# Kernel tuning notes

Hardware: AMD Instinct MI355X
Metric: run time of the kernel (lower is better)

## Reference

```python
import jax, jax.numpy as jnp
import numpy as np

B, NQ, NK = 16, 512, 1024
CQ, CV = 128, 128
H, D = 8, 64            # nb_heads, attention_size
SCALE = float(np.sqrt(D))


def setup_inputs() -> dict:
    key = jax.random.key(0)
    ks = jax.random.split(key, 10)
    s = 0.02
    return {
        "query": jax.random.normal(ks[0], (B, NQ, CQ), jnp.float32),
        "key": jax.random.normal(ks[1], (B, NK, CV), jnp.float32),
        "c_mask": jax.random.randint(ks[2], (B, NK), 0, 2).astype(jnp.float32),
        # torch Linear params, stored as [in, out] so y = x @ W + b
        "Wq": jax.random.normal(ks[3], (CQ, H * D), jnp.float32) * s,
        "bq": jnp.zeros((H * D,), jnp.float32),
        "Wk": jax.random.normal(ks[4], (CV, H * D), jnp.float32) * s,
        "bk": jnp.zeros((H * D,), jnp.float32),
        "Wv": jax.random.normal(ks[5], (CV, H * D), jnp.float32) * s,
        "bv": jnp.zeros((H * D,), jnp.float32),
    }


def reference(query, key, c_mask, Wq, bq, Wk, bk, Wv, bv):
    # projections -> [B, N, H, D]
    q = (query @ Wq + bq).reshape(B, NQ, H, D)
    k = (key @ Wk + bk).reshape(B, NK, H, D)
    v = (key @ Wv + bv).reshape(B, NK, H, D)
    # scaled scores [B, H, NQ, NK]
    scores = jnp.einsum('bqhd,bkhd->bhqk', q / SCALE, k)
    # additive mask: c_mask [B, NK] broadcasts over heads and queries
    scores = scores - 100000.0 * (1.0 - c_mask[:, None, None, :])
    attn = jax.nn.softmax(scores, axis=-1)
    # weighted values -> [B, NQ, H, D] -> concat heads
    c = jnp.einsum('bhqk,bkhd->bqhd', attn, v)
    return c.reshape(B, NQ, H * D)
```

## Files before the change

kernel.cpp:

```cpp
#include <hip/hip_runtime.h>
#include <hip/hip_bf16.h>

#define B_  16
#define NQ_ 512
#define NK_ 1024
#define CQ_ 128
#define H_  8
#define D_  64
#define HD_ 512

typedef __attribute__((ext_vector_type(8))) short short8;
typedef __attribute__((ext_vector_type(4))) float floatx4;

__device__ __forceinline__ short f2bf(float f) {
    union { float f; unsigned u; } x; x.f = f;
    unsigned r = (x.u + 0x7fffu + ((x.u >> 16) & 1u)) >> 16;
    return (short)r;
}
__device__ __forceinline__ int f2bf_pk(float a, float b) {
    __hip_bfloat162 h = __float22bfloat162_rn(make_float2(a, b));
    int r; __builtin_memcpy(&r, &h, 4); return r;
}
__device__ __forceinline__ short8 pack8(float4 a, float4 b) {
    union { int4 i; short8 s; } u;
    u.i = make_int4(f2bf_pk(a.x, a.y), f2bf_pk(a.z, a.w),
                    f2bf_pk(b.x, b.y), f2bf_pk(b.z, b.w));
    return u.s;
}
__device__ __forceinline__ int2 packi2(floatx4 a) {
    return make_int2(f2bf_pk(a[0], a[1]), f2bf_pk(a[2], a[3]));
}
__device__ __forceinline__ void async16(const short* g, short* l) {
    __builtin_amdgcn_global_load_lds(
        (const __attribute__((address_space(1))) void*)g,
        (__attribute__((address_space(3))) void*)l, 16, 0, 0);
}

__global__ void prep_kernel(const float* __restrict__ W0, const float* __restrict__ W1,
                            const float* __restrict__ W2, short* __restrict__ T0,
                            short* __restrict__ T1, short* __restrict__ T2,
                            const float* __restrict__ bq, float* __restrict__ bqs,
                            float qscale) {
    int gi = blockIdx.x * blockDim.x + threadIdx.x;
    if (gi < 196608) {
        int sel = gi >> 16;
        int idx = gi & 65535;
        const float* W = sel == 0 ? W0 : (sel == 1 ? W1 : W2);
        short* T = sel == 0 ? T0 : (sel == 1 ? T1 : T2);
        float s = sel == 0 ? qscale : 1.0f;
        int n = idx >> 7, k = idx & 127;
        T[idx] = f2bf(W[k * HD_ + n] * s);
        return;
    }
    int j = gi - 196608;
    if (j < HD_) bqs[j] = bq[j] * qscale;
}

__global__ __launch_bounds__(256, 2) void kvproj_kernel(
    const float* __restrict__ key_,
    const short* __restrict__ wkt, const short* __restrict__ wvt,
    const float* __restrict__ bk, const float* __restrict__ bv,
    short* __restrict__ ks, short* __restrict__ vt)
{
    __shared__ __align__(16) short csh[9216];

    int bx = blockIdx.x;
    const short* Wt; const float* bias; short* out; int transposed;
    if (bx < 128) { Wt = wkt; bias = bk; out = ks; transposed = 0; }
    else { bx -= 128; Wt = wvt; bias = bv; out = vt; transposed = 1; }

    const int tid  = threadIdx.x;
    const int w    = tid >> 6, lane = tid & 63;
    const int l15  = lane & 15, quad = lane >> 4;
    const int mbase = bx * 128;

    short8 afr[2][4];
    #pragma unroll
    for (int mt = 0; mt < 2; ++mt) {
        const float* xrow = key_ + (size_t)(mbase + w * 32 + mt * 16 + l15) * CQ_;
        #pragma unroll
        for (int kt = 0; kt < 4; ++kt)
            afr[mt][kt] = pack8(*(const float4*)(xrow + kt * 32 + quad * 8),
                                *(const float4*)(xrow + kt * 32 + quad * 8 + 4));
    }

    const int b  = mbase >> 10;
    const int r0 = mbase & 1023;

    #pragma unroll
    for (int hh = 0; hh < 2; ++hh) {
        const int h = blockIdx.y * 2 + hh;
        short8 bfr[4][4];
        #pragma unroll
        for (int nt = 0; nt < 4; ++nt) {
            const short8* wrow = (const short8*)(Wt + (size_t)(h * 64 + nt * 16 + l15) * CQ_);
            #pragma unroll
            for (int kt = 0; kt < 4; ++kt) bfr[nt][kt] = wrow[kt * 4 + quad];
        }
        floatx4 acc[2][4];
        #pragma unroll
        for (int mt = 0; mt < 2; ++mt)
            #pragma unroll
            for (int nt = 0; nt < 4; ++nt) {
                floatx4 a = {0.f, 0.f, 0.f, 0.f};
                #pragma unroll
                for (int kt = 0; kt < 4; ++kt)
                    a = __builtin_amdgcn_mfma_f32_16x16x32_bf16(afr[mt][kt], bfr[nt][kt], a, 0, 0, 0);
                acc[mt][nt] = a;
            }
        __syncthreads();
        #pragma unroll
        for (int mt = 0; mt < 2; ++mt)
            #pragma unroll
            for (int nt = 0; nt < 4; ++nt) {
                const float bvv = bias[h * 64 + nt * 16 + l15];
                #pragma unroll
                for (int i = 0; i < 4; ++i) {
                    const short s = f2bf(acc[mt][nt][i] + bvv);
                    const int m = w * 32 + mt * 16 + quad * 4 + i;
                    const int n = nt * 16 + l15;
                    if (!transposed) csh[m * 72 + n]  = s;
                    else             csh[n * 136 + m] = s;
                }
            }
        __syncthreads();

        const size_t bh = (size_t)(b * H_ + h);
        if (!transposed) {
            short* dst = out + (bh * NK_ + r0) * D_;
            #pragma unroll
            for (int it = 0; it < 4; ++it) {
                const int idx = it * 256 + tid;
                const int row = idx >> 3, c8 = (idx & 7) * 8;
                *(short8*)(dst + idx * 8) = *(const short8*)&csh[row * 72 + c8];
            }
        } else {
            short* dst = out + bh * D_ * NK_ + r0;
            #pragma unroll
            for (int it = 0; it < 4; ++it) {
                const int idx = it * 256 + tid;
                const int row = idx >> 4, c8 = (idx & 15) * 8;
                *(short8*)(dst + (size_t)row * NK_ + c8) = *(const short8*)&csh[row * 136 + c8];
            }
        }
    }
}

__global__ __launch_bounds__(256, 2) void attn_kernel(
    const float* __restrict__ query, const short* __restrict__ ks,
    const short* __restrict__ vt, const float* __restrict__ cmask,
    const short* __restrict__ wqt, const float* __restrict__ bqs,
    float* __restrict__ out)
{
    __shared__ __align__(16) short kbuf[2][64 * 64];
    __shared__ __align__(16) short vbuf[2][64 * 64];
    __shared__ __align__(16) short psh[128 * 64];

    const int tid = threadIdx.x;
    const int w = tid >> 6, lane = tid & 63;
    const int l15 = lane & 15, quad = lane >> 4;

    const int bx   = blockIdx.x;
    const int bh_i = bx & 127;
    const int qq   = bx >> 7;
    const int h    = bh_i & 7;
    const int b    = bh_i >> 3;

    const size_t bh = (size_t)bh_i;
    const short* kb_ = ks + bh * NK_ * D_;
    const short* vb  = vt + bh * D_ * NK_;
    const float* mk  = cmask + (size_t)b * NK_;

    short8 qa[2][2];
    {
        short8 waf[4][4];
        #pragma unroll
        for (int dt = 0; dt < 4; ++dt)
            #pragma unroll
            for (int kt = 0; kt < 4; ++kt)
                waf[dt][kt] = *(const short8*)(wqt + (size_t)(h * 64 + dt * 16 + l15) * CQ_ + kt * 32 + quad * 8);
        const int qr0 = qq * 128 + w * 32;
        #pragma unroll
        for (int g = 0; g < 2; ++g) {
            const float* qrow = query + ((size_t)b * NQ_ + qr0 + g * 16 + l15) * CQ_;
            short8 bqf[4];
            #pragma unroll
            for (int kt = 0; kt < 4; ++kt)
                bqf[kt] = pack8(*(const float4*)(qrow + kt * 32 + quad * 8),
                                *(const float4*)(qrow + kt * 32 + quad * 8 + 4));
            const int prow = w * 32 + g * 16 + l15;
            #pragma unroll
            for (int dt = 0; dt < 4; ++dt) {
                float4 bi = *(const float4*)(bqs + h * 64 + dt * 16 + quad * 4);
                floatx4 a = {bi.x, bi.y, bi.z, bi.w};
                #pragma unroll
                for (int kt = 0; kt < 4; ++kt)
                    a = __builtin_amdgcn_mfma_f32_16x16x32_bf16(waf[dt][kt], bqf[kt], a, 0, 0, 0);
                const int c16 = (dt * 2 + (quad >> 1)) ^ (prow & 7);
                *(int2*)&psh[prow * 64 + c16 * 8 + (quad & 1) * 4] = packi2(a);
            }
            qa[g][0] = *(const short8*)&psh[prow * 64 + ((quad    ) ^ (prow & 7)) * 8];
            qa[g][1] = *(const short8*)&psh[prow * 64 + ((4 + quad) ^ (prow & 7)) * 8];
        }
    }

    const int srow8 = lane >> 3, sc = lane & 7;

    float l_lane[2] = {0.f, 0.f};
    floatx4 o_acc[2][4];
    #pragma unroll
    for (int g = 0; g < 2; ++g)
        #pragma unroll
        for (int dt = 0; dt < 4; ++dt) o_acc[g][dt] = (floatx4){0.f, 0.f, 0.f, 0.f};

    #pragma unroll
    for (int j = 0; j < 2; ++j) {
        const int row = w * 16 + j * 8 + srow8;
        const int cs = sc ^ (row & 7);
        async16(kb_ + (size_t)row * D_ + cs * 8, &kbuf[0][(w * 16 + j * 8) * 64]);
        async16(vb + (size_t)row * NK_ + cs * 8, &vbuf[0][(w * 16 + j * 8) * 64]);
    }
    __syncthreads();

    for (int t = 0; t < 16; ++t) {
        const int cur = t & 1;
        if (t < 15) {
            const int nb = (t + 1) * 64, nxt = cur ^ 1;
            #pragma unroll
            for (int j = 0; j < 2; ++j) {
                const int row = w * 16 + j * 8 + srow8;
                const int cs = sc ^ (row & 7);
                async16(kb_ + (size_t)(nb + row) * D_ + cs * 8, &kbuf[nxt][(w * 16 + j * 8) * 64]);
                async16(vb + (size_t)row * NK_ + nb + cs * 8, &vbuf[nxt][(w * 16 + j * 8) * 64]);
            }
        }
        const short* kb = kbuf[cur];
        const short* vbl = vbuf[cur];
        const int kbase = t * 64;

        short8 ka[4][2];
        #pragma unroll
        for (int nt = 0; nt < 4; ++nt) {
            const int row = nt * 16 + l15;
            ka[nt][0] = *(const short8*)&kb[row * 64 + ((quad    ) ^ (row & 7)) * 8];
            ka[nt][1] = *(const short8*)&kb[row * 64 + ((4 + quad) ^ (row & 7)) * 8];
        }
        short8 vf[2][4];
        #pragma unroll
        for (int dt = 0; dt < 4; ++dt) {
            const int row = dt * 16 + l15;
            vf[0][dt] = *(const short8*)&vbl[row * 64 + ((quad    ) ^ (row & 7)) * 8];
            vf[1][dt] = *(const short8*)&vbl[row * 64 + ((4 + quad) ^ (row & 7)) * 8];
        }
        float4 m4[4];
        #pragma unroll
        for (int nt = 0; nt < 4; ++nt)
            m4[nt] = *(const float4*)(mk + kbase + nt * 16 + quad * 4);

        #pragma unroll
        for (int g = 0; g < 2; ++g) {
            floatx4 st[4];
            #pragma unroll
            for (int nt = 0; nt < 4; ++nt) {
                floatx4 a = {0.f, 0.f, 0.f, 0.f};
                a = __builtin_amdgcn_mfma_f32_16x16x32_bf16(ka[nt][1], qa[g][1], a, 0, 0, 0);
                a = __builtin_amdgcn_mfma_f32_16x16x32_bf16(ka[nt][0], qa[g][0], a, 0, 0, 0);
                st[nt] = a;
            }
            const int prow = w * 32 + g * 16 + l15;
            float psum = 0.f;
            #pragma unroll
            for (int nt = 0; nt < 4; ++nt) {
                float p0 = m4[nt].x * __builtin_amdgcn_exp2f(st[nt][0]);
                float p1 = m4[nt].y * __builtin_amdgcn_exp2f(st[nt][1]);
                float p2 = m4[nt].z * __builtin_amdgcn_exp2f(st[nt][2]);
                float p3 = m4[nt].w * __builtin_amdgcn_exp2f(st[nt][3]);
                psum += (p0 + p1) + (p2 + p3);
                int2 pk = make_int2(f2bf_pk(p0, p1), f2bf_pk(p2, p3));
                const int c16 = (2 * nt + (quad >> 1)) ^ (prow & 7);
                *(int2*)&psh[prow * 64 + c16 * 8 + (quad & 1) * 4] = pk;
            }
            l_lane[g] += psum;
            #pragma unroll
            for (int kt = 0; kt < 2; ++kt) {
                short8 pa = *(const short8*)&psh[prow * 64 + ((kt * 4 + quad) ^ (prow & 7)) * 8];
                #pragma unroll
                for (int dt = 0; dt < 4; ++dt)
                    o_acc[g][dt] = __builtin_amdgcn_mfma_f32_16x16x32_bf16(vf[kt][dt], pa, o_acc[g][dt], 0, 0, 0);
            }
        }
        __syncthreads();
    }

    #pragma unroll
    for (int g = 0; g < 2; ++g) {
        float ls = l_lane[g];
        ls += __shfl_xor(ls, 16);
        ls += __shfl_xor(ls, 32);
        const float linv = 1.0f / ls;
        const int qr = qq * 128 + w * 32 + g * 16 + l15;
        float* orow = out + ((size_t)b * NQ_ + qr) * HD_ + h * D_;
        #pragma unroll
        for (int dt = 0; dt < 4; ++dt) {
            float4 v = make_float4(o_acc[g][dt][0] * linv, o_acc[g][dt][1] * linv,
                                   o_acc[g][dt][2] * linv, o_acc[g][dt][3] * linv);
            *(float4*)(orow + dt * 16 + quad * 4) = v;
        }
    }
}

extern "C" void kernel_launch(void* const* d_in, const int* in_sizes, int n_in,
                              void* d_out, int out_size, void* d_ws, size_t ws_size,
                              hipStream_t stream) {
    const float* query = (const float*)d_in[0];
    const float* key   = (const float*)d_in[1];
    const float* cmask = (const float*)d_in[2];
    const float* Wq    = (const float*)d_in[3];
    const float* bq    = (const float*)d_in[4];
    const float* Wk    = (const float*)d_in[5];
    const float* bk    = (const float*)d_in[6];
    const float* Wv    = (const float*)d_in[7];
    const float* bv    = (const float*)d_in[8];
    float* out = (float*)d_out;

    char* ws = (char*)d_ws;
    short* ks  = (short*)(ws);
    short* vt  = (short*)(ws + (size_t)(16u << 20));
    char*  w32 = ws + (size_t)(32u << 20);
    short* wqt = (short*)(w32);
    short* wkt = (short*)(w32 + 131072);
    short* wvt = (short*)(w32 + 131072 * 2);
    float* bqs = (float*)(w32 + 131072 * 3);

    const float qscale = 0.125f * 1.44269504f;
    prep_kernel<<<dim3(771), dim3(256), 0, stream>>>(
        Wq, Wk, Wv, wqt, wkt, wvt, bq, bqs, qscale);

    kvproj_kernel<<<dim3(256, 4), dim3(256), 0, stream>>>(
        key, wkt, wvt, bk, bv, ks, vt);

    attn_kernel<<<dim3(512), dim3(256), 0, stream>>>(
        query, ks, vt, cmask, wqt, bqs, out);
}
```

Measured before the change: 147.6 us.

## Tile weight transpose via LDS, widen kvproj heads, stage 128-key chunks

The weight prep kernel now reads each weight matrix with coalesced float4 loads, transposes it through LDS and writes 16-byte rows, replacing the strided scalar gather. The K/V projection kernel processes four heads per block instead of two, halving the grid and reusing the converted key fragments across more heads. The attention kernel stages two 64-key sub-tiles per pipeline phase, doubling the LDS K/V buffers so there are half as many barriers per block. The larger LDS footprint may lower attention occupancy, and the smaller kvproj grid gives less parallelism.

```diff
diff --git a/kernel.cpp b/kernel.cpp
--- a/kernel.cpp
+++ b/kernel.cpp
@@ -36,24 +36,42 @@
         (__attribute__((address_space(3))) void*)l, 16, 0, 0);
 }
 
-__global__ void prep_kernel(const float* __restrict__ W0, const float* __restrict__ W1,
-                            const float* __restrict__ W2, short* __restrict__ T0,
-                            short* __restrict__ T1, short* __restrict__ T2,
-                            const float* __restrict__ bq, float* __restrict__ bqs,
-                            float qscale) {
-    int gi = blockIdx.x * blockDim.x + threadIdx.x;
-    if (gi < 196608) {
-        int sel = gi >> 16;
-        int idx = gi & 65535;
-        const float* W = sel == 0 ? W0 : (sel == 1 ? W1 : W2);
-        short* T = sel == 0 ? T0 : (sel == 1 ? T1 : T2);
-        float s = sel == 0 ? qscale : 1.0f;
-        int n = idx >> 7, k = idx & 127;
-        T[idx] = f2bf(W[k * HD_ + n] * s);
+__global__ __launch_bounds__(256) void prep_kernel(
+    const float* __restrict__ W0, const float* __restrict__ W1,
+    const float* __restrict__ W2, short* __restrict__ T0,
+    short* __restrict__ T1, short* __restrict__ T2,
+    const float* __restrict__ bq, float* __restrict__ bqs, float qscale)
+{
+    const int blk = blockIdx.x, t = threadIdx.x;
+    if (blk == 48) {
+        bqs[t]       = bq[t] * qscale;
+        bqs[t + 256] = bq[t + 256] * qscale;
         return;
     }
-    int j = gi - 196608;
-    if (j < HD_) bqs[j] = bq[j] * qscale;
+    __shared__ short tsh[32 * 132];
+    const int mat = blk >> 4, nb = blk & 15;
+    const float* W = mat == 0 ? W0 : (mat == 1 ? W1 : W2);
+    short* T = mat == 0 ? T0 : (mat == 1 ? T1 : T2);
+    const float s = mat == 0 ? qscale : 1.0f;
+
+    #pragma unroll
+    for (int i = 0; i < 4; ++i) {
+        const int idx = i * 256 + t;
+        const int k = idx >> 3, c = (idx & 7) * 4;
+        float4 v = *(const float4*)(W + (size_t)k * HD_ + nb * 32 + c);
+        tsh[(c + 0) * 132 + k] = f2bf(v.x * s);
+        tsh[(c + 1) * 132 + k] = f2bf(v.y * s);
+        tsh[(c + 2) * 132 + k] = f2bf(v.z * s);
+        tsh[(c + 3) * 132 + k] = f2bf(v.w * s);
+    }
+    __syncthreads();
+    #pragma unroll
+    for (int j = 0; j < 2; ++j) {
+        const int idx = j * 256 + t;
+        const int n = idx >> 4, seg = (idx & 15) * 8;
+        *(short8*)(T + (size_t)(nb * 32 + n) * CQ_ + seg) =
+            *(const short8*)&tsh[n * 132 + seg];
+    }
 }
 
 __global__ __launch_bounds__(256, 2) void kvproj_kernel(
@@ -88,8 +106,8 @@
     const int r0 = mbase & 1023;
 
     #pragma unroll
-    for (int hh = 0; hh < 2; ++hh) {
-        const int h = blockIdx.y * 2 + hh;
+    for (int hh = 0; hh < 4; ++hh) {
+        const int h = blockIdx.y * 4 + hh;
         short8 bfr[4][4];
         #pragma unroll
         for (int nt = 0; nt < 4; ++nt) {
@@ -152,8 +170,8 @@
     const short* __restrict__ wqt, const float* __restrict__ bqs,
     float* __restrict__ out)
 {
-    __shared__ __align__(16) short kbuf[2][64 * 64];
-    __shared__ __align__(16) short vbuf[2][64 * 64];
+    __shared__ __align__(16) short kbuf[2][2][64 * 64];
+    __shared__ __align__(16) short vbuf[2][2][64 * 64];
     __shared__ __align__(16) short psh[128 * 64];
 
     const int tid = threadIdx.x;
@@ -205,88 +223,90 @@
     }
 
     const int srow8 = lane >> 3, sc = lane & 7;
-
-    float l_lane[2] = {0.f, 0.f};
-    floatx4 o_acc[2][4];
-    #pragma unroll
-    for (int g = 0; g < 2; ++g)
-        #pragma unroll
-        for (int dt = 0; dt < 4; ++dt) o_acc[g][dt] = (floatx4){0.f, 0.f, 0.f, 0.f};
-
-    #pragma unroll
-    for (int j = 0; j < 2; ++j) {
-        const int row = w * 16 + j * 8 + srow8;
-        const int cs = sc ^ (row & 7);
-        async16(kb_ + (size_t)row * D_ + cs * 8, &kbuf[0][(w * 16 + j * 8) * 64]);
-        async16(vb + (size_t)row * NK_ + cs * 8, &vbuf[0][(w * 16 + j * 8) * 64]);
-    }
-    __syncthreads();
-
-    for (int t = 0; t < 16; ++t) {
-        const int cur = t & 1;
-        if (t < 15) {
-            const int nb = (t + 1) * 64, nxt = cur ^ 1;
+    auto stage = [&](int kb0, short (*kdst)[4096], short (*vdst)[4096]) {
+        #pragma unroll
+        for (int sub = 0; sub < 2; ++sub)
             #pragma unroll
             for (int j = 0; j < 2; ++j) {
                 const int row = w * 16 + j * 8 + srow8;
                 const int cs = sc ^ (row & 7);
-                async16(kb_ + (size_t)(nb + row) * D_ + cs * 8, &kbuf[nxt][(w * 16 + j * 8) * 64]);
-                async16(vb + (size_t)row * NK_ + nb + cs * 8, &vbuf[nxt][(w * 16 + j * 8) * 64]);
-            }
-        }
-        const short* kb = kbuf[cur];
-        const short* vbl = vbuf[cur];
-        const int kbase = t * 64;
-
-        short8 ka[4][2];
-        #pragma unroll
-        for (int nt = 0; nt < 4; ++nt) {
-            const int row = nt * 16 + l15;
-            ka[nt][0] = *(const short8*)&kb[row * 64 + ((quad    ) ^ (row & 7)) * 8];
-            ka[nt][1] = *(const short8*)&kb[row * 64 + ((4 + quad) ^ (row & 7)) * 8];
-        }
-        short8 vf[2][4];
-        #pragma unroll
-        for (int dt = 0; dt < 4; ++dt) {
-            const int row = dt * 16 + l15;
-            vf[0][dt] = *(const short8*)&vbl[row * 64 + ((quad    ) ^ (row & 7)) * 8];
-            vf[1][dt] = *(const short8*)&vbl[row * 64 + ((4 + quad) ^ (row & 7)) * 8];
-        }
-        float4 m4[4];
-        #pragma unroll
-        for (int nt = 0; nt < 4; ++nt)
-            m4[nt] = *(const float4*)(mk + kbase + nt * 16 + quad * 4);
-
-        #pragma unroll
-        for (int g = 0; g < 2; ++g) {
-            floatx4 st[4];
+                async16(kb_ + (size_t)(kb0 + sub * 64 + row) * D_ + cs * 8,
+                        &kdst[sub][(w * 16 + j * 8) * 64]);
+                async16(vb + (size_t)row * NK_ + kb0 + sub * 64 + cs * 8,
+                        &vdst[sub][(w * 16 + j * 8) * 64]);
+            }
+    };
+
+    float l_lane[2] = {0.f, 0.f};
+    floatx4 o_acc[2][4];
+    #pragma unroll
+    for (int g = 0; g < 2; ++g)
+        #pragma unroll
+        for (int dt = 0; dt < 4; ++dt) o_acc[g][dt] = (floatx4){0.f, 0.f, 0.f, 0.f};
+
+    stage(0, kbuf[0], vbuf[0]);
+    __syncthreads();
+
+    for (int ph = 0; ph < 8; ++ph) {
+        const int cur = ph & 1;
+        if (ph < 7) stage((ph + 1) * 128, kbuf[cur ^ 1], vbuf[cur ^ 1]);
+
+        #pragma unroll
+        for (int sub = 0; sub < 2; ++sub) {
+            const short* kb  = kbuf[cur][sub];
+            const short* vbl = vbuf[cur][sub];
+            const int kbase = ph * 128 + sub * 64;
+
+            short8 ka[4][2];
             #pragma unroll
             for (int nt = 0; nt < 4; ++nt) {
-                floatx4 a = {0.f, 0.f, 0.f, 0.f};
-                a = __builtin_amdgcn_mfma_f32_16x16x32_bf16(ka[nt][1], qa[g][1], a, 0, 0, 0);
-                a = __builtin_amdgcn_mfma_f32_16x16x32_bf16(ka[nt][0], qa[g][0], a, 0, 0, 0);
-                st[nt] = a;
-            }
-            const int prow = w * 32 + g * 16 + l15;
-            float psum = 0.f;
-            #pragma unroll
-            for (int nt = 0; nt < 4; ++nt) {
-                float p0 = m4[nt].x * __builtin_amdgcn_exp2f(st[nt][0]);
-                float p1 = m4[nt].y * __builtin_amdgcn_exp2f(st[nt][1]);
-                float p2 = m4[nt].z * __builtin_amdgcn_exp2f(st[nt][2]);
-                float p3 = m4[nt].w * __builtin_amdgcn_exp2f(st[nt][3]);
-                psum += (p0 + p1) + (p2 + p3);
-                int2 pk = make_int2(f2bf_pk(p0, p1), f2bf_pk(p2, p3));
-                const int c16 = (2 * nt + (quad >> 1)) ^ (prow & 7);
-                *(int2*)&psh[prow * 64 + c16 * 8 + (quad & 1) * 4] = pk;
-            }
-            l_lane[g] += psum;
-            #pragma unroll
-            for (int kt = 0; kt < 2; ++kt) {
-                short8 pa = *(const short8*)&psh[prow * 64 + ((kt * 4 + quad) ^ (prow & 7)) * 8];
-                #pragma unroll
-                for (int dt = 0; dt < 4; ++dt)
-                    o_acc[g][dt] = __builtin_amdgcn_mfma_f32_16x16x32_bf16(vf[kt][dt], pa, o_acc[g][dt], 0, 0, 0);
+                const int row = nt * 16 + l15;
+                ka[nt][0] = *(const short8*)&kb[row * 64 + ((quad    ) ^ (row & 7)) * 8];
+                ka[nt][1] = *(const short8*)&kb[row * 64 + ((4 + quad) ^ (row & 7)) * 8];
+            }
+            short8 vf[2][4];
+            #pragma unroll
+            for (int dt = 0; dt < 4; ++dt) {
+                const int row = dt * 16 + l15;
+                vf[0][dt] = *(const short8*)&vbl[row * 64 + ((quad    ) ^ (row & 7)) * 8];
+                vf[1][dt] = *(const short8*)&vbl[row * 64 + ((4 + quad) ^ (row & 7)) * 8];
+            }
+            float4 m4[4];
+            #pragma unroll
+            for (int nt = 0; nt < 4; ++nt)
+                m4[nt] = *(const float4*)(mk + kbase + nt * 16 + quad * 4);
+
+            #pragma unroll
+            for (int g = 0; g < 2; ++g) {
+                floatx4 st[4];
+                #pragma unroll
+                for (int nt = 0; nt < 4; ++nt) {
+                    floatx4 a = {0.f, 0.f, 0.f, 0.f};
+                    a = __builtin_amdgcn_mfma_f32_16x16x32_bf16(ka[nt][1], qa[g][1], a, 0, 0, 0);
+                    a = __builtin_amdgcn_mfma_f32_16x16x32_bf16(ka[nt][0], qa[g][0], a, 0, 0, 0);
+                    st[nt] = a;
+                }
+                const int prow = w * 32 + g * 16 + l15;
+                float psum = 0.f;
+                #pragma unroll
+                for (int nt = 0; nt < 4; ++nt) {
+                    float p0 = m4[nt].x * __builtin_amdgcn_exp2f(st[nt][0]);
+                    float p1 = m4[nt].y * __builtin_amdgcn_exp2f(st[nt][1]);
+                    float p2 = m4[nt].z * __builtin_amdgcn_exp2f(st[nt][2]);
+                    float p3 = m4[nt].w * __builtin_amdgcn_exp2f(st[nt][3]);
+                    psum += (p0 + p1) + (p2 + p3);
+                    int2 pk = make_int2(f2bf_pk(p0, p1), f2bf_pk(p2, p3));
+                    const int c16 = (2 * nt + (quad >> 1)) ^ (prow & 7);
+                    *(int2*)&psh[prow * 64 + c16 * 8 + (quad & 1) * 4] = pk;
+                }
+                l_lane[g] += psum;
+                #pragma unroll
+                for (int kt = 0; kt < 2; ++kt) {
+                    short8 pa = *(const short8*)&psh[prow * 64 + ((kt * 4 + quad) ^ (prow & 7)) * 8];
+                    #pragma unroll
+                    for (int dt = 0; dt < 4; ++dt)
+                        o_acc[g][dt] = __builtin_amdgcn_mfma_f32_16x16x32_bf16(vf[kt][dt], pa, o_acc[g][dt], 0, 0, 0);
+                }
             }
         }
         __syncthreads();
@@ -333,10 +353,10 @@
     float* bqs = (float*)(w32 + 131072 * 3);
 
     const float qscale = 0.125f * 1.44269504f;
-    prep_kernel<<<dim3(771), dim3(256), 0, stream>>>(
+    prep_kernel<<<dim3(49), dim3(256), 0, stream>>>(
         Wq, Wk, Wv, wqt, wkt, wvt, bq, bqs, qscale);
 
-    kvproj_kernel<<<dim3(256, 4), dim3(256), 0, stream>>>(
+    kvproj_kernel<<<dim3(256, 2), dim3(256), 0, stream>>>(
         key, wkt, wvt, bk, bv, ks, vt);
 
     attn_kernel<<<dim3(512), dim3(256), 0, stream>>>(
```

Result: no change. 146.7 us (-0.6%).
